# Kernel optimization log

Measured on AMD Instinct MI355X. Metric: run time of the kernel, lower is better.

Reference implementation:

```python
import jax, jax.numpy as jnp
import numpy as np

NEG_SLOPE = 0.15


def _gcn_norm(edge_index, num_nodes):
    # PyG GCNConv default: add self-loops, symmetric normalization.
    src = jnp.concatenate([edge_index[0], jnp.arange(num_nodes)])
    dst = jnp.concatenate([edge_index[1], jnp.arange(num_nodes)])
    deg = jax.ops.segment_sum(jnp.ones_like(src, dtype=jnp.float32), dst,
                              num_segments=num_nodes)
    dis = jnp.where(deg > 0, jax.lax.rsqrt(jnp.maximum(deg, 1.0)), 0.0)
    norm = dis[src] * dis[dst]  # [E + N]
    return src, dst, norm


def _gcn_conv(h, W, b, src, dst, norm, num_nodes):
    h = h @ W                                   # dense transform first (PyG order)
    msg = h[src] * norm[:, None]                # gather + scale per edge
    out = jax.ops.segment_sum(msg, dst, num_segments=num_nodes)  # scatter-add
    return out + b


def setup_inputs() -> dict:
    key = jax.random.key(0)
    ks = jax.random.split(key, 16)
    N, E, D = 20000, 320000, 128
    x = jax.random.normal(ks[0], (N, D), dtype=jnp.float32)
    edge_index = jax.random.randint(ks[1], (2, E), 0, N, dtype=jnp.int32)
    edge_attr = jax.random.normal(ks[2], (E, 2), dtype=jnp.float32)

    def lin(k, fi, fo):
        kw, kb = jax.random.split(k)
        s = 1.0 / np.sqrt(fi)
        return (jax.random.uniform(kw, (fi, fo), jnp.float32, -s, s),
                jax.random.uniform(kb, (fo,), jnp.float32, -s, s))

    W1, b1 = lin(ks[3], D, 512)
    W2, b2 = lin(ks[4], 512, 256)
    W3, b3 = lin(ks[5], 256, 128)
    Wp, bp = lin(ks[6], 128, 16)   # pre_fc (128 -> 16)
    Wf1, bf1 = lin(ks[7], 16, 32)  # fallback MLP classifier
    Wf2, bf2 = lin(ks[8], 32, 2)
    return {"x": x, "edge_index": edge_index, "edge_attr": edge_attr,
            "W1": W1, "b1": b1, "W2": W2, "b2": b2, "W3": W3, "b3": b3,
            "Wp": Wp, "bp": bp, "Wf1": Wf1, "bf1": bf1, "Wf2": Wf2, "bf2": bf2}


def reference(x, edge_index, edge_attr, W1, b1, W2, b2, W3, b3,
              Wp, bp, Wf1, bf1, Wf2, bf2):
    N = x.shape[0]
    src, dst, norm = _gcn_norm(edge_index, N)
    lrelu = lambda h: jax.nn.leaky_relu(h, NEG_SLOPE)
    h = lrelu(_gcn_conv(x, W1, b1, src, dst, norm, N))   # dropout = identity (eval)
    h = lrelu(_gcn_conv(h, W2, b2, src, dst, norm, N))
    h = lrelu(_gcn_conv(h, W3, b3, src, dst, norm, N))
    h = h @ Wp + bp                                      # pre_fc: 128 -> 16
    h = lrelu(h @ Wf1 + bf1)                             # classifier MLP
    return h @ Wf2 + bf2                                 # [N, 2]
```

## Files before the change

### kernel.cpp

```cpp
#include <hip/hip_runtime.h>
#include <hip/hip_bf16.h>

typedef __hip_bfloat16 bf16;
typedef unsigned short ushort_t;
typedef __attribute__((ext_vector_type(8))) short short8v;
typedef __attribute__((ext_vector_type(4))) float floatx4;

#define NEG_SLOPE 0.15f

__device__ __forceinline__ float us2f(unsigned short u) {
    unsigned int x = ((unsigned int)u) << 16;
    float f;
    __builtin_memcpy(&f, &x, 4);
    return f;
}
__device__ __forceinline__ unsigned short f2us(float v) {
    bf16 h = __float2bfloat16(v);
    unsigned short u;
    __builtin_memcpy(&u, &h, 2);
    return u;
}

#define GLOAD_LDS16(gp, lp)                                                  \
    __builtin_amdgcn_global_load_lds(                                        \
        (const __attribute__((address_space(1))) unsigned int*)(gp),         \
        (__attribute__((address_space(3))) unsigned int*)(lp), 16, 0, 0)

__device__ __forceinline__ int block_flag(const unsigned int* __restrict__ xw) {
    __shared__ int cnt;
    if (threadIdx.x == 0) cnt = 0;
    __syncthreads();
    if (threadIdx.x < 256) {
        unsigned int w = xw[threadIdx.x];
        unsigned int e = (w >> 7) & 0xFF;
        if ((w & 0xFFFF) == 0 || (e >= 100 && e <= 140)) atomicAdd(&cnt, 1);
    }
    __syncthreads();
    return cnt >= 150;
}

struct PrepDesc {
    const void* src[14];
    void* dst[14];
    int n[14];
    int K[14], Nn[14];
};

__global__ void prep_small_kernel(PrepDesc d, const void* __restrict__ xsrc) {
    int f = block_flag((const unsigned int*)xsrc);
    int t = blockIdx.y;
    int Kt = d.K[t];
    int nt = d.n[t];
    if (Kt == -2) {
        ushort_t* out = (ushort_t*)d.dst[t];
        const void* in = d.src[t];
        int stride = gridDim.x * blockDim.x;
        for (int i = blockIdx.x * blockDim.x + threadIdx.x; i < nt; i += stride)
            out[i] = f ? ((const unsigned short*)in)[i] : f2us(((const float*)in)[i]);
        return;
    }
    int i = blockIdx.x * blockDim.x + threadIdx.x;
    if (i >= nt) return;
    if (Kt == -1) {
        ((int*)d.dst[t])[i] = 0;
    } else if (Kt == 0) {
        ((float*)d.dst[t])[i] = f ? us2f(((const unsigned short*)d.src[t])[i])
                                  : ((const float*)d.src[t])[i];
    } else {
        int K = Kt, Nn = d.Nn[t];
        int n = i / K, k = i - n * K;
        size_t si = (size_t)k * Nn + n;
        ((ushort_t*)d.dst[t])[i] = f ? ((const unsigned short*)d.src[t])[si]
                                     : f2us(((const float*)d.src[t])[si]);
    }
}

__global__ void count_deg_kernel(const int* __restrict__ dst, int* __restrict__ deg,
                                 int E, int N) {
    int i = blockIdx.x * blockDim.x + threadIdx.x;
    if (i < E) {
        int d = dst[i];
        d = d < 0 ? 0 : (d >= N ? N - 1 : d);
        atomicAdd(&deg[d], 1);
    }
}

__global__ void scan_merged_kernel(const int* __restrict__ deg, int* __restrict__ offsets,
                                   int* __restrict__ cursor, float* __restrict__ dis,
                                   int* __restrict__ bsumf, int N) {
    __shared__ int sh[1024];
    __shared__ int base_s;
    int tid = threadIdx.x;
    int b = blockIdx.x;
    int i = b * 1024 + tid;
    int v = (i < N) ? (deg[i] + 1) : 0;
    sh[tid] = v;
    __syncthreads();
    for (int off = 1; off < 1024; off <<= 1) {
        int t = (tid >= off) ? sh[tid - off] : 0;
        __syncthreads();
        sh[tid] += t;
        __syncthreads();
    }
    if (tid == 0) {
        __hip_atomic_store(&bsumf[b], sh[1023] + 1, __ATOMIC_RELEASE,
                           __HIP_MEMORY_SCOPE_AGENT);
        int a = 0;
        for (int pb = 0; pb < b; ++pb) {
            int val;
            do {
                val = __hip_atomic_load(&bsumf[pb], __ATOMIC_ACQUIRE,
                                        __HIP_MEMORY_SCOPE_AGENT);
            } while (val == 0);
            a += val - 1;
        }
        base_s = a;
    }
    __syncthreads();
    if (i < N) {
        int base = base_s;
        int d = deg[i] + 1;
        int inc = sh[tid];
        int excl = base + inc - d;
        offsets[i] = excl;
        cursor[i] = excl;
        dis[i] = rsqrtf((float)d);
        if (i == N - 1) offsets[N] = base + inc;
    }
}

__global__ void fill_csr_kernel(const int* __restrict__ src, const int* __restrict__ dst,
                                const float* __restrict__ dis, int* __restrict__ cursor,
                                int2* __restrict__ edges, int E, int N, int Etot) {
    int i = blockIdx.x * blockDim.x + threadIdx.x;
    int s, d;
    if (i < E) { s = src[i]; d = dst[i]; }
    else if (i < Etot) { s = d = i - E; }
    else return;
    s = s < 0 ? 0 : (s >= N ? N - 1 : s);
    d = d < 0 ? 0 : (d >= N ? N - 1 : d);
    int pos = atomicAdd(&cursor[d], 1);
    if (pos >= 0 && pos < Etot) edges[pos] = make_int2(s, __float_as_int(dis[s]));
}

template <int VEC> struct LdT;
template <> struct LdT<2> { typedef unsigned int T; };
template <> struct LdT<4> { typedef uint2 T; };

template <int VEC>
__device__ __forceinline__ void addv(typename LdT<VEC>::T u, float w, float* acc);
template <>
__device__ __forceinline__ void addv<2>(unsigned int u, float w, float* acc) {
    acc[0] += w * us2f((unsigned short)(u & 0xFFFF));
    acc[1] += w * us2f((unsigned short)(u >> 16));
}
template <>
__device__ __forceinline__ void addv<4>(uint2 u, float w, float* acc) {
    acc[0] += w * us2f((unsigned short)(u.x & 0xFFFF));
    acc[1] += w * us2f((unsigned short)(u.x >> 16));
    acc[2] += w * us2f((unsigned short)(u.y & 0xFFFF));
    acc[3] += w * us2f((unsigned short)(u.y >> 16));
}

template <int VEC, int NB>
__device__ __forceinline__ void edge_block(
    int2 ed, int j0, int cnt,
    const ushort_t* __restrict__ Hin, int fo, int N, float* acc) {
    typedef typename LdT<VEC>::T LT;
    const int F = VEC * 64;
    float w[NB];
    LT u[NB];
#pragma unroll
    for (int j = 0; j < NB; ++j) {
        int s = __builtin_amdgcn_readlane(ed.x, j0 + j);
        int wb = __builtin_amdgcn_readlane(ed.y, j0 + j);
        s = s < 0 ? 0 : (s >= N ? N - 1 : s);
        if (cnt >= 0 && j0 + j >= cnt) wb = 0;
        w[j] = __int_as_float(wb);
        u[j] = *(const LT*)(Hin + (size_t)s * F + fo);
    }
#pragma unroll
    for (int j = 0; j < NB; ++j) addv<VEC>(u[j], w[j], acc);
}

template <int VEC>
__device__ __forceinline__ void agg_core(
    const ushort_t* __restrict__ Hin, const int* __restrict__ offsets,
    const int2* __restrict__ edges, const float* __restrict__ dis,
    int node, int lane, int N, int Etot,
    const float* __restrict__ bias, int do_lrelu, float* outv) {
    const int F = VEC * 64;
    node = __builtin_amdgcn_readfirstlane(node);
    int beg = offsets[node], end = offsets[node + 1];
    beg = beg < 0 ? 0 : (beg > Etot ? Etot : beg);
    end = end < beg ? beg : (end > Etot ? Etot : end);

    float acc[VEC];
#pragma unroll
    for (int v = 0; v < VEC; ++v) acc[v] = 0.f;

    int fo = lane * VEC;

    for (int e0 = beg; e0 < end; e0 += 64) {
        int idx = e0 + lane;
        idx = idx <= Etot - 1 ? idx : Etot - 1;
        int2 ed = edges[idx];
        int cnt = end - e0;
        cnt = cnt > 64 ? 64 : cnt;
        int j0 = 0;
        for (; j0 + 16 <= cnt; j0 += 16)
            edge_block<VEC, 16>(ed, j0, -1, Hin, fo, N, acc);
        if (j0 + 8 <= cnt) {
            edge_block<VEC, 8>(ed, j0, -1, Hin, fo, N, acc);
            j0 += 8;
        }
        if (j0 < cnt)
            edge_block<VEC, 8>(ed, j0, cnt, Hin, fo, N, acc);
    }

    float dn = dis[node];
#pragma unroll
    for (int v = 0; v < VEC; ++v) {
        float a = acc[v] * dn;
        if (bias) a += bias[fo + v];
        if (do_lrelu) a = (a > 0.f) ? a : a * NEG_SLOPE;
        outv[v] = a;
    }
}

template <int VEC>
__global__ __launch_bounds__(256) void agg_kernel(
    const ushort_t* __restrict__ Hin, ushort_t* __restrict__ OutB,
    const int* __restrict__ offsets, const int2* __restrict__ edges,
    const float* __restrict__ dis, int N, int Etot,
    const float* __restrict__ bias, int do_lrelu) {
    int lane = threadIdx.x & 63;
    int node = blockIdx.x * 4 + (threadIdx.x >> 6);
    if (node >= N) return;
    float outv[VEC];
    agg_core<VEC>(Hin, offsets, edges, dis, node, lane, N, Etot, bias, do_lrelu, outv);
    size_t base = (size_t)node * (VEC * 64) + lane * VEC;
    if (VEC == 2) {
        unsigned int w = ((unsigned int)f2us(outv[1]) << 16) | f2us(outv[0]);
        *(unsigned int*)(OutB + base) = w;
    } else {
        uint2 w;
        w.x = ((unsigned int)f2us(outv[1]) << 16) | f2us(outv[0]);
        w.y = ((unsigned int)f2us(outv[3]) << 16) | f2us(outv[2]);
        *(uint2*)(OutB + base) = w;
    }
}

__global__ __launch_bounds__(256) void agg_head_kernel(
    const ushort_t* __restrict__ Hin,
    const int* __restrict__ offsets, const int2* __restrict__ edges,
    const float* __restrict__ dis, int N, int Etot,
    const float* __restrict__ b3,
    const float* __restrict__ Wp, const float* __restrict__ bp,
    const float* __restrict__ Wf1, const float* __restrict__ bf1v,
    const float* __restrict__ Wf2, const float* __restrict__ bf2v,
    void* __restrict__ out, const void* __restrict__ xsrc) {
    int flag = block_flag((const unsigned int*)xsrc);
    int lane = threadIdx.x & 63;
    int node = blockIdx.x * 4 + (threadIdx.x >> 6);
    if (node >= N) return;
    float h[2];
    agg_core<2>(Hin, offsets, edges, dis, node, lane, N, Etot, b3, 1, h);

    int fo = lane * 2;
    float p[16];
#pragma unroll
    for (int j = 0; j < 16; ++j)
        p[j] = h[0] * Wp[fo * 16 + j] + h[1] * Wp[(fo + 1) * 16 + j];
#pragma unroll
    for (int m = 1; m < 64; m <<= 1) {
#pragma unroll
        for (int j = 0; j < 16; ++j) p[j] += __shfl_xor(p[j], m, 64);
    }
    float a0 = 0.f, a1 = 0.f;
    if (lane < 32) {
        float s = bf1v[lane];
#pragma unroll
        for (int k = 0; k < 16; ++k) s += (p[k] + bp[k]) * Wf1[k * 32 + lane];
        s = (s > 0.f) ? s : s * NEG_SLOPE;
        a0 = s * Wf2[lane * 2 + 0];
        a1 = s * Wf2[lane * 2 + 1];
    }
#pragma unroll
    for (int m = 1; m < 64; m <<= 1) {
        a0 += __shfl_xor(a0, m, 64);
        a1 += __shfl_xor(a1, m, 64);
    }
    if (lane == 0) {
        float o0 = a0 + bf2v[0];
        float o1 = a1 + bf2v[1];
        if (flag) {
            unsigned int w = ((unsigned int)f2us(o1) << 16) | f2us(o0);
            *(unsigned int*)((ushort_t*)out + (size_t)node * 2) = w;
        } else {
            *(float2*)((float*)out + (size_t)node * 2) = make_float2(o0, o1);
        }
    }
}

__global__ __launch_bounds__(256) void mfma_gemm_kernel(
    const ushort_t* __restrict__ A, const ushort_t* __restrict__ Bt,
    ushort_t* __restrict__ C,
    int M, int K, int Nn, const float* __restrict__ bias, int do_lrelu) {
    __shared__ ushort_t As[128 * 64];
    __shared__ ushort_t Bs[64 * 64];

    int tid = threadIdx.x;
    int row0 = blockIdx.y * 128;
    int col0 = blockIdx.x * 64;
    int lane = tid & 63;
    int w = tid >> 6;
    int quad = lane >> 4;
    int col = lane & 15;
    int wr = (w >> 1) * 64;
    int wc = (w & 1) * 32;

    floatx4 acc[4][2];
#pragma unroll
    for (int i = 0; i < 4; ++i)
#pragma unroll
        for (int j = 0; j < 2; ++j) acc[i][j] = (floatx4){0.f, 0.f, 0.f, 0.f};

    int aoff[4], boff[2];
#pragma unroll
    for (int rt = 0; rt < 4; ++rt) {
        int r = wr + rt * 16 + col;
        aoff[rt] = (r * 128 + quad * 16) ^ ((r & 7) << 4);
    }
#pragma unroll
    for (int ct = 0; ct < 2; ++ct) {
        int r = wc + ct * 16 + col;
        boff[ct] = (r * 128 + quad * 16) ^ ((r & 7) << 4);
    }

    for (int k0 = 0; k0 < K; k0 += 64) {
#pragma unroll
        for (int i = 0; i < 4; ++i) {
            int t = i * 256 + tid;
            int r = t >> 3;
            int g = (t & 7) ^ (r & 7);
            const ushort_t* src = A + (size_t)(row0 + r) * K + k0 + g * 8;
            GLOAD_LDS16(src, &As[t * 8]);
        }
#pragma unroll
        for (int i = 0; i < 2; ++i) {
            int t = i * 256 + tid;
            int r = t >> 3;
            int g = (t & 7) ^ (r & 7);
            const ushort_t* src = Bt + (size_t)(col0 + r) * K + k0 + g * 8;
            GLOAD_LDS16(src, &Bs[t * 8]);
        }
        __syncthreads();

#pragma unroll
        for (int ks = 0; ks < 2; ++ks) {
            short8v af[4], bf[2];
#pragma unroll
            for (int rt = 0; rt < 4; ++rt)
                af[rt] = *(const short8v*)((const char*)As + (aoff[rt] ^ (ks * 64)));
#pragma unroll
            for (int ct = 0; ct < 2; ++ct)
                bf[ct] = *(const short8v*)((const char*)Bs + (boff[ct] ^ (ks * 64)));
#pragma unroll
            for (int rt = 0; rt < 4; ++rt)
#pragma unroll
                for (int ct = 0; ct < 2; ++ct)
                    acc[rt][ct] = __builtin_amdgcn_mfma_f32_16x16x32_bf16(
                        af[rt], bf[ct], acc[rt][ct], 0, 0, 0);
        }
        __syncthreads();
    }

#pragma unroll
    for (int rt = 0; rt < 4; ++rt) {
#pragma unroll
        for (int ct = 0; ct < 2; ++ct) {
            int gcol = col0 + wc + ct * 16 + col;
            float bv = bias ? bias[gcol] : 0.f;
#pragma unroll
            for (int r = 0; r < 4; ++r) {
                int grow = row0 + wr + rt * 16 + quad * 4 + r;
                if (grow >= M) continue;
                float v = acc[rt][ct][r] + bv;
                if (do_lrelu) v = (v > 0.f) ? v : v * NEG_SLOPE;
                C[(size_t)grow * Nn + gcol] = f2us(v);
            }
        }
    }
}

extern "C" void kernel_launch(void* const* d_in, const int* in_sizes, int n_in,
                              void* d_out, int out_size, void* d_ws, size_t ws_size,
                              hipStream_t stream) {
    const int* ei = (const int*)d_in[1];

    const int N = in_sizes[0] / 128;
    const int E = in_sizes[1] / 2;
    const int Etot = E + N;
    const int nb = (N + 1023) / 1024;
    const int* srcv = ei;
    const int* dstv = ei + E;

    uintptr_t p = (uintptr_t)d_ws;
    auto alloc = [&](size_t bytes) -> void* {
        p = (p + 255) & ~(uintptr_t)255;
        void* r = (void*)p;
        p += bytes;
        return r;
    };
    int*      deg     = (int*)alloc((size_t)(N + nb + 1) * 4);
    int*      bsumf   = deg + N;
    int*      offsets = (int*)alloc((size_t)(N + 1) * 4);
    int*      cursor  = (int*)alloc((size_t)N * 4);
    float*    dis     = (float*)alloc((size_t)N * 4);
    int2*     edges   = (int2*)alloc((size_t)Etot * 8);
    ushort_t* xb      = (ushort_t*)alloc((size_t)N * 128 * 2);

    const int K1 = 128, N1 = 512, K2 = 512, N2 = 256, K3 = 256, N3 = 128;
    ushort_t* W1t = (ushort_t*)alloc((size_t)K1 * N1 * 2);
    ushort_t* W2t = (ushort_t*)alloc((size_t)K2 * N2 * 2);
    ushort_t* W3t = (ushort_t*)alloc((size_t)K3 * N3 * 2);

    float* smalls[9];
    const int wmap[9] = {4, 6, 8, 9, 10, 11, 12, 13, 14};
    for (int t = 0; t < 9; ++t)
        smalls[t] = (float*)alloc((size_t)in_sizes[wmap[t]] * 4);
    const float *b1 = smalls[0], *b2 = smalls[1], *b3 = smalls[2];
    const float *Wp = smalls[3], *bp = smalls[4];
    const float *Wf1 = smalls[5], *bf1v = smalls[6];
    const float *Wf2 = smalls[7], *bf2v = smalls[8];

    ushort_t* BufT0 = (ushort_t*)alloc((size_t)N * 128 * 2);
    ushort_t* BufH1 = (ushort_t*)alloc((size_t)N * 512 * 2);
    ushort_t* BufT2 = (ushort_t*)alloc((size_t)N * 256 * 2);
    ushort_t* t0 = BufT0;
    ushort_t* t3 = BufT0;
    ushort_t* H1 = BufH1;
    ushort_t* H2 = BufH1;
    ushort_t* t2 = BufT2;

    {
        PrepDesc pd;
        for (int t = 0; t < 9; ++t) {
            pd.src[t] = d_in[wmap[t]];
            pd.dst[t] = smalls[t];
            pd.n[t] = in_sizes[wmap[t]];
            pd.K[t] = 0; pd.Nn[t] = 0;
        }
        pd.src[9]  = d_in[3]; pd.dst[9]  = W1t; pd.n[9]  = K1 * N1; pd.K[9]  = K1; pd.Nn[9]  = N1;
        pd.src[10] = d_in[5]; pd.dst[10] = W2t; pd.n[10] = K2 * N2; pd.K[10] = K2; pd.Nn[10] = N2;
        pd.src[11] = d_in[7]; pd.dst[11] = W3t; pd.n[11] = K3 * N3; pd.K[11] = K3; pd.Nn[11] = N3;
        pd.src[12] = nullptr; pd.dst[12] = deg; pd.n[12] = N + nb + 1; pd.K[12] = -1; pd.Nn[12] = 0;
        pd.src[13] = d_in[0]; pd.dst[13] = xb;  pd.n[13] = N * 128;    pd.K[13] = -2; pd.Nn[13] = 0;
        dim3 g((K2 * N2 + 255) / 256, 14);
        prep_small_kernel<<<g, 256, 0, stream>>>(pd, d_in[0]);
    }

    count_deg_kernel<<<(E + 255) / 256, 256, 0, stream>>>(dstv, deg, E, N);
    scan_merged_kernel<<<nb, 1024, 0, stream>>>(deg, offsets, cursor, dis, bsumf, N);
    fill_csr_kernel<<<(Etot + 255) / 256, 256, 0, stream>>>(srcv, dstv, dis, cursor,
                                                            edges, E, N, Etot);

    int aggGrid = (N + 3) / 4;
    agg_kernel<2><<<aggGrid, 256, 0, stream>>>(xb, t0, offsets, edges, dis,
                                               N, Etot, nullptr, 0);
    {
        dim3 g(N1 / 64, (N + 127) / 128);
        mfma_gemm_kernel<<<g, 256, 0, stream>>>(t0, W1t, H1, N, K1, N1, b1, 1);
    }
    {
        dim3 g(N2 / 64, (N + 127) / 128);
        mfma_gemm_kernel<<<g, 256, 0, stream>>>(H1, W2t, t2, N, K2, N2, nullptr, 0);
    }
    agg_kernel<4><<<aggGrid, 256, 0, stream>>>(t2, H2, offsets, edges, dis,
                                               N, Etot, b2, 1);
    {
        dim3 g(N3 / 64, (N + 127) / 128);
        mfma_gemm_kernel<<<g, 256, 0, stream>>>(H2, W3t, t3, N, K3, N3, nullptr, 0);
    }
    agg_head_kernel<<<aggGrid, 256, 0, stream>>>(t3, offsets, edges, dis, N, Etot,
                                                 b3, Wp, bp, Wf1, bf1v, Wf2, bf2v,
                                                 d_out, d_in[0]);
}
```

Before: 259.2 us.

## Process two nodes per wavefront in aggregation and fold degree count into prep

Each aggregation wavefront now handles two destination nodes and interleaves their gather loads, issuing both nodes' 8-edge loads before consuming them, to raise memory-level parallelism. The grid is halved to match. The degree histogram is moved into the prep kernel as a grid-stride task, with degrees zeroed by a memset beforehand, which removes one kernel launch. In exchange, per-thread register use and divergence from unequal node degrees go up, and the fixed 16-edge unroll is replaced by 8-edge blocks.

```diff
diff --git a/kernel.cpp b/kernel.cpp
--- a/kernel.cpp
+++ b/kernel.cpp
@@ -51,6 +51,18 @@
     int t = blockIdx.y;
     int Kt = d.K[t];
     int nt = d.n[t];
+    if (Kt == -3) {
+        const int* dstv = (const int*)d.src[t];
+        int* deg = (int*)d.dst[t];
+        int Nn = d.Nn[t];
+        int stride = gridDim.x * blockDim.x;
+        for (int i = blockIdx.x * blockDim.x + threadIdx.x; i < nt; i += stride) {
+            int dd = dstv[i];
+            dd = dd < 0 ? 0 : (dd >= Nn ? Nn - 1 : dd);
+            atomicAdd(&deg[dd], 1);
+        }
+        return;
+    }
     if (Kt == -2) {
         ushort_t* out = (ushort_t*)d.dst[t];
         const void* in = d.src[t];
@@ -61,9 +73,7 @@
     }
     int i = blockIdx.x * blockDim.x + threadIdx.x;
     if (i >= nt) return;
-    if (Kt == -1) {
-        ((int*)d.dst[t])[i] = 0;
-    } else if (Kt == 0) {
+    if (Kt == 0) {
         ((float*)d.dst[t])[i] = f ? us2f(((const unsigned short*)d.src[t])[i])
                                   : ((const float*)d.src[t])[i];
     } else {
@@ -72,16 +82,6 @@
         size_t si = (size_t)k * Nn + n;
         ((ushort_t*)d.dst[t])[i] = f ? ((const unsigned short*)d.src[t])[si]
                                      : f2us(((const float*)d.src[t])[si]);
-    }
-}
-
-__global__ void count_deg_kernel(const int* __restrict__ dst, int* __restrict__ deg,
-                                 int E, int N) {
-    int i = blockIdx.x * blockDim.x + threadIdx.x;
-    if (i < E) {
-        int d = dst[i];
-        d = d < 0 ? 0 : (d >= N ? N - 1 : d);
-        atomicAdd(&deg[d], 1);
     }
 }
 
@@ -163,68 +163,100 @@
 }
 
 template <int VEC, int NB>
-__device__ __forceinline__ void edge_block(
+struct EB {
+    typename LdT<VEC>::T u[NB];
+    float w[NB];
+};
+
+template <int VEC, int NB>
+__device__ __forceinline__ void edge_issue(
     int2 ed, int j0, int cnt,
-    const ushort_t* __restrict__ Hin, int fo, int N, float* acc) {
-    typedef typename LdT<VEC>::T LT;
+    const ushort_t* __restrict__ Hin, int fo, int N, EB<VEC, NB>& b) {
     const int F = VEC * 64;
-    float w[NB];
-    LT u[NB];
 #pragma unroll
     for (int j = 0; j < NB; ++j) {
         int s = __builtin_amdgcn_readlane(ed.x, j0 + j);
         int wb = __builtin_amdgcn_readlane(ed.y, j0 + j);
         s = s < 0 ? 0 : (s >= N ? N - 1 : s);
-        if (cnt >= 0 && j0 + j >= cnt) wb = 0;
-        w[j] = __int_as_float(wb);
-        u[j] = *(const LT*)(Hin + (size_t)s * F + fo);
-    }
-#pragma unroll
-    for (int j = 0; j < NB; ++j) addv<VEC>(u[j], w[j], acc);
+        if (j0 + j >= cnt) wb = 0;
+        b.w[j] = __int_as_float(wb);
+        b.u[j] = *(const typename LdT<VEC>::T*)(Hin + (size_t)s * F + fo);
+    }
+}
+template <int VEC, int NB>
+__device__ __forceinline__ void edge_consume(const EB<VEC, NB>& b, float* acc) {
+#pragma unroll
+    for (int j = 0; j < NB; ++j) addv<VEC>(b.u[j], b.w[j], acc);
 }
 
 template <int VEC>
-__device__ __forceinline__ void agg_core(
+__device__ __forceinline__ void agg_core_dual(
     const ushort_t* __restrict__ Hin, const int* __restrict__ offsets,
     const int2* __restrict__ edges, const float* __restrict__ dis,
-    int node, int lane, int N, int Etot,
-    const float* __restrict__ bias, int do_lrelu, float* outv) {
-    const int F = VEC * 64;
-    node = __builtin_amdgcn_readfirstlane(node);
-    int beg = offsets[node], end = offsets[node + 1];
-    beg = beg < 0 ? 0 : (beg > Etot ? Etot : beg);
-    end = end < beg ? beg : (end > Etot ? Etot : end);
-
-    float acc[VEC];
-#pragma unroll
-    for (int v = 0; v < VEC; ++v) acc[v] = 0.f;
+    int nodeA, int nodeB, int lane, int N, int Etot,
+    const float* __restrict__ bias, int do_lrelu, float* outA, float* outB) {
+    nodeA = __builtin_amdgcn_readfirstlane(nodeA);
+    nodeB = __builtin_amdgcn_readfirstlane(nodeB);
+    bool hasB = nodeB < N;
+    int begA = offsets[nodeA], endA = offsets[nodeA + 1];
+    int begB = hasB ? offsets[nodeB] : 0;
+    int endB = hasB ? offsets[nodeB + 1] : 0;
+    begA = begA < 0 ? 0 : (begA > Etot ? Etot : begA);
+    endA = endA < begA ? begA : (endA > Etot ? Etot : endA);
+    begB = begB < 0 ? 0 : (begB > Etot ? Etot : begB);
+    endB = endB < begB ? begB : (endB > Etot ? Etot : endB);
+
+    float accA[VEC], accB[VEC];
+#pragma unroll
+    for (int v = 0; v < VEC; ++v) { accA[v] = 0.f; accB[v] = 0.f; }
 
     int fo = lane * VEC;
-
-    for (int e0 = beg; e0 < end; e0 += 64) {
-        int idx = e0 + lane;
-        idx = idx <= Etot - 1 ? idx : Etot - 1;
-        int2 ed = edges[idx];
-        int cnt = end - e0;
-        cnt = cnt > 64 ? 64 : cnt;
-        int j0 = 0;
-        for (; j0 + 16 <= cnt; j0 += 16)
-            edge_block<VEC, 16>(ed, j0, -1, Hin, fo, N, acc);
-        if (j0 + 8 <= cnt) {
-            edge_block<VEC, 8>(ed, j0, -1, Hin, fo, N, acc);
-            j0 += 8;
-        }
-        if (j0 < cnt)
-            edge_block<VEC, 8>(ed, j0, cnt, Hin, fo, N, acc);
-    }
-
-    float dn = dis[node];
+    int eA = begA, eB = begB;
+    while (eA < endA || eB < endB) {
+        int cntA = endA - eA; cntA = cntA < 0 ? 0 : (cntA > 64 ? 64 : cntA);
+        int cntB = endB - eB; cntB = cntB < 0 ? 0 : (cntB > 64 ? 64 : cntB);
+        int2 edA = make_int2(0, 0), edB = make_int2(0, 0);
+        if (cntA) { int ia = eA + lane; ia = ia <= Etot - 1 ? ia : Etot - 1; edA = edges[ia]; }
+        if (cntB) { int ib = eB + lane; ib = ib <= Etot - 1 ? ib : Etot - 1; edB = edges[ib]; }
+        int cmax = cntA > cntB ? cntA : cntB;
+        for (int j0 = 0; j0 < cmax; j0 += 8) {
+            bool dA = j0 < cntA, dB = j0 < cntB;
+            EB<VEC, 8> A, B;
+            if (dA) edge_issue<VEC, 8>(edA, j0, cntA, Hin, fo, N, A);
+            if (dB) edge_issue<VEC, 8>(edB, j0, cntB, Hin, fo, N, B);
+            if (dA) edge_consume<VEC, 8>(A, accA);
+            if (dB) edge_consume<VEC, 8>(B, accB);
+        }
+        eA += cntA; eB += cntB;
+    }
+
+    float dnA = dis[nodeA];
+    float dnB = hasB ? dis[nodeB] : 0.f;
 #pragma unroll
     for (int v = 0; v < VEC; ++v) {
-        float a = acc[v] * dn;
-        if (bias) a += bias[fo + v];
-        if (do_lrelu) a = (a > 0.f) ? a : a * NEG_SLOPE;
-        outv[v] = a;
+        float a = accA[v] * dnA;
+        float b = accB[v] * dnB;
+        if (bias) { a += bias[fo + v]; b += bias[fo + v]; }
+        if (do_lrelu) {
+            a = (a > 0.f) ? a : a * NEG_SLOPE;
+            b = (b > 0.f) ? b : b * NEG_SLOPE;
+        }
+        outA[v] = a; outB[v] = b;
+    }
+}
+
+template <int VEC>
+__device__ __forceinline__ void agg_store(ushort_t* __restrict__ OutB_, int node,
+                                          int lane, const float* outv) {
+    size_t base = (size_t)node * (VEC * 64) + lane * VEC;
+    if (VEC == 2) {
+        unsigned int w = ((unsigned int)f2us(outv[1]) << 16) | f2us(outv[0]);
+        *(unsigned int*)(OutB_ + base) = w;
+    } else {
+        uint2 w;
+        w.x = ((unsigned int)f2us(outv[1]) << 16) | f2us(outv[0]);
+        w.y = ((unsigned int)f2us(outv[3]) << 16) | f2us(outv[2]);
+        *(uint2*)(OutB_ + base) = w;
     }
 }
 
@@ -235,19 +267,55 @@
     const float* __restrict__ dis, int N, int Etot,
     const float* __restrict__ bias, int do_lrelu) {
     int lane = threadIdx.x & 63;
-    int node = blockIdx.x * 4 + (threadIdx.x >> 6);
-    if (node >= N) return;
-    float outv[VEC];
-    agg_core<VEC>(Hin, offsets, edges, dis, node, lane, N, Etot, bias, do_lrelu, outv);
-    size_t base = (size_t)node * (VEC * 64) + lane * VEC;
-    if (VEC == 2) {
-        unsigned int w = ((unsigned int)f2us(outv[1]) << 16) | f2us(outv[0]);
-        *(unsigned int*)(OutB + base) = w;
-    } else {
-        uint2 w;
-        w.x = ((unsigned int)f2us(outv[1]) << 16) | f2us(outv[0]);
-        w.y = ((unsigned int)f2us(outv[3]) << 16) | f2us(outv[2]);
-        *(uint2*)(OutB + base) = w;
+    int wv = blockIdx.x * 4 + (threadIdx.x >> 6);
+    int nodeA = wv * 2, nodeB = wv * 2 + 1;
+    if (nodeA >= N) return;
+    float oA[VEC], oB[VEC];
+    agg_core_dual<VEC>(Hin, offsets, edges, dis, nodeA, nodeB, lane, N, Etot,
+                       bias, do_lrelu, oA, oB);
+    agg_store<VEC>(OutB, nodeA, lane, oA);
+    if (nodeB < N) agg_store<VEC>(OutB, nodeB, lane, oB);
+}
+
+__device__ __forceinline__ void head_mlp(
+    const float* h, int lane, int node, int flag,
+    const float* __restrict__ Wp, const float* __restrict__ bp,
+    const float* __restrict__ Wf1, const float* __restrict__ bf1v,
+    const float* __restrict__ Wf2, const float* __restrict__ bf2v,
+    void* __restrict__ out) {
+    int fo = lane * 2;
+    float p[16];
+#pragma unroll
+    for (int j = 0; j < 16; ++j)
+        p[j] = h[0] * Wp[fo * 16 + j] + h[1] * Wp[(fo + 1) * 16 + j];
+#pragma unroll
+    for (int m = 1; m < 64; m <<= 1) {
+#pragma unroll
+        for (int j = 0; j < 16; ++j) p[j] += __shfl_xor(p[j], m, 64);
+    }
+    float a0 = 0.f, a1 = 0.f;
+    if (lane < 32) {
+        float s = bf1v[lane];
+#pragma unroll
+        for (int k = 0; k < 16; ++k) s += (p[k] + bp[k]) * Wf1[k * 32 + lane];
+        s = (s > 0.f) ? s : s * NEG_SLOPE;
+        a0 = s * Wf2[lane * 2 + 0];
+        a1 = s * Wf2[lane * 2 + 1];
+    }
+#pragma unroll
+    for (int m = 1; m < 64; m <<= 1) {
+        a0 += __shfl_xor(a0, m, 64);
+        a1 += __shfl_xor(a1, m, 64);
+    }
+    if (lane == 0) {
+        float o0 = a0 + bf2v[0];
+        float o1 = a1 + bf2v[1];
+        if (flag) {
+            unsigned int w = ((unsigned int)f2us(o1) << 16) | f2us(o0);
+            *(unsigned int*)((ushort_t*)out + (size_t)node * 2) = w;
+        } else {
+            *(float2*)((float*)out + (size_t)node * 2) = make_float2(o0, o1);
+        }
     }
 }
 
@@ -262,45 +330,15 @@
     void* __restrict__ out, const void* __restrict__ xsrc) {
     int flag = block_flag((const unsigned int*)xsrc);
     int lane = threadIdx.x & 63;
-    int node = blockIdx.x * 4 + (threadIdx.x >> 6);
-    if (node >= N) return;
-    float h[2];
-    agg_core<2>(Hin, offsets, edges, dis, node, lane, N, Etot, b3, 1, h);
-
-    int fo = lane * 2;
-    float p[16];
-#pragma unroll
-    for (int j = 0; j < 16; ++j)
-        p[j] = h[0] * Wp[fo * 16 + j] + h[1] * Wp[(fo + 1) * 16 + j];
-#pragma unroll
-    for (int m = 1; m < 64; m <<= 1) {
-#pragma unroll
-        for (int j = 0; j < 16; ++j) p[j] += __shfl_xor(p[j], m, 64);
-    }
-    float a0 = 0.f, a1 = 0.f;
-    if (lane < 32) {
-        float s = bf1v[lane];
-#pragma unroll
-        for (int k = 0; k < 16; ++k) s += (p[k] + bp[k]) * Wf1[k * 32 + lane];
-        s = (s > 0.f) ? s : s * NEG_SLOPE;
-        a0 = s * Wf2[lane * 2 + 0];
-        a1 = s * Wf2[lane * 2 + 1];
-    }
-#pragma unroll
-    for (int m = 1; m < 64; m <<= 1) {
-        a0 += __shfl_xor(a0, m, 64);
-        a1 += __shfl_xor(a1, m, 64);
-    }
-    if (lane == 0) {
-        float o0 = a0 + bf2v[0];
-        float o1 = a1 + bf2v[1];
-        if (flag) {
-            unsigned int w = ((unsigned int)f2us(o1) << 16) | f2us(o0);
-            *(unsigned int*)((ushort_t*)out + (size_t)node * 2) = w;
-        } else {
-            *(float2*)((float*)out + (size_t)node * 2) = make_float2(o0, o1);
-        }
-    }
+    int wv = blockIdx.x * 4 + (threadIdx.x >> 6);
+    int nodeA = wv * 2, nodeB = wv * 2 + 1;
+    if (nodeA >= N) return;
+    float hA[2], hB[2];
+    agg_core_dual<2>(Hin, offsets, edges, dis, nodeA, nodeB, lane, N, Etot,
+                     b3, 1, hA, hB);
+    head_mlp(hA, lane, nodeA, flag, Wp, bp, Wf1, bf1v, Wf2, bf2v, out);
+    if (nodeB < N)
+        head_mlp(hB, lane, nodeB, flag, Wp, bp, Wf1, bf1v, Wf2, bf2v, out);
 }
 
 __global__ __launch_bounds__(256) void mfma_gemm_kernel(
@@ -444,6 +482,8 @@
     ushort_t* H2 = BufH1;
     ushort_t* t2 = BufT2;
 
+    hipMemsetAsync(deg, 0, (size_t)(N + nb + 1) * 4, stream);
+
     {
         PrepDesc pd;
         for (int t = 0; t < 9; ++t) {
@@ -455,18 +495,17 @@
         pd.src[9]  = d_in[3]; pd.dst[9]  = W1t; pd.n[9]  = K1 * N1; pd.K[9]  = K1; pd.Nn[9]  = N1;
         pd.src[10] = d_in[5]; pd.dst[10] = W2t; pd.n[10] = K2 * N2; pd.K[10] = K2; pd.Nn[10] = N2;
         pd.src[11] = d_in[7]; pd.dst[11] = W3t; pd.n[11] = K3 * N3; pd.K[11] = K3; pd.Nn[11] = N3;
-        pd.src[12] = nullptr; pd.dst[12] = deg; pd.n[12] = N + nb + 1; pd.K[12] = -1; pd.Nn[12] = 0;
-        pd.src[13] = d_in[0]; pd.dst[13] = xb;  pd.n[13] = N * 128;    pd.K[13] = -2; pd.Nn[13] = 0;
+        pd.src[12] = dstv;    pd.dst[12] = deg; pd.n[12] = E;       pd.K[12] = -3; pd.Nn[12] = N;
+        pd.src[13] = d_in[0]; pd.dst[13] = xb;  pd.n[13] = N * 128; pd.K[13] = -2; pd.Nn[13] = 0;
         dim3 g((K2 * N2 + 255) / 256, 14);
         prep_small_kernel<<<g, 256, 0, stream>>>(pd, d_in[0]);
     }
 
-    count_deg_kernel<<<(E + 255) / 256, 256, 0, stream>>>(dstv, deg, E, N);
     scan_merged_kernel<<<nb, 1024, 0, stream>>>(deg, offsets, cursor, dis, bsumf, N);
     fill_csr_kernel<<<(Etot + 255) / 256, 256, 0, stream>>>(srcv, dstv, dis, cursor,
                                                             edges, E, N, Etot);
 
-    int aggGrid = (N + 3) / 4;
+    int aggGrid = (N + 7) / 8;
     agg_kernel<2><<<aggGrid, 256, 0, stream>>>(xb, t0, offsets, edges, dis,
                                                N, Etot, nullptr, 0);
     {
```

Result: slower. 269.3 us (+3.9%).
